# Performance work log

Hardware: AMD Instinct MI355X
Metric: run time of the kernel (lower is better)

Reference implementation:

```python
import jax, jax.numpy as jnp
import numpy as np

N = 50000        # nodes (== input_dim, featureless layer)
E = 400000       # edges in sparse support
HID = 200        # hidden dim hardcoded in GCN
NUM_CLASSES = 10


def setup_inputs() -> dict:
    key = jax.random.key(0)
    k1, k2, k3, k4 = jax.random.split(key, 4)
    return {
        "x": jnp.zeros((N, 1), dtype=jnp.float32),  # unused (featureless layer1)
        "support_rows": jax.random.randint(k1, (E,), 0, N, dtype=jnp.int32),
        "support_cols": jax.random.randint(k2, (E,), 0, N, dtype=jnp.int32),
        "support_vals": jax.random.uniform(k3, (E,), dtype=jnp.float32),
        "W0": jax.random.normal(k4, (N, HID), dtype=jnp.float32),
        "W2": jax.random.normal(jax.random.fold_in(key, 5), (HID, NUM_CLASSES), dtype=jnp.float32),
    }


def reference(x, support_rows, support_cols, support_vals, W0, W2):
    # Layer 1 (featureless): pre_sup = W0; out = A @ W0 via sparse edge list.
    # SpMM as gather + scale + segment-sum:
    gathered = W0[support_cols] * support_vals[:, None]          # [E, HID]
    h = jax.ops.segment_sum(gathered, support_rows, num_segments=N)  # [N, HID]
    h = jax.nn.relu(h)
    # Layer 2 (SimpleGraphConvolution, no act, no bias): h @ W2
    return h @ W2                                                # [N, NUM_CLASSES]
```

## Files before the change

kernel.cpp:

```cpp
#include <hip/hip_runtime.h>

#define N_NODES 50000
#define N_EDGES 400000
#define HID     200
#define NCLS    10
#define SLOTS   40


__device__ __forceinline__ unsigned bf16rn(float f) {
    unsigned u = __float_as_uint(f);
    return (u + 0x7FFFu + ((u >> 16) & 1u)) >> 16;
}
__device__ __forceinline__ float bl(unsigned u) { return __uint_as_float(u << 16); }
__device__ __forceinline__ float bh(unsigned u) { return __uint_as_float(u & 0xFFFF0000u); }

__global__ __launch_bounds__(256) void k_convert(const float4* __restrict__ W04,
                                                 uint4* __restrict__ W0h4,
                                                 int4* __restrict__ cnt4) {
    int i = blockIdx.x * 256 + threadIdx.x;
    if (i < 12504) cnt4[i] = make_int4(0, 0, 0, 0);
    if (i >= (N_NODES * HID) / 8) return;
    float4 f0 = W04[i * 2];
    float4 f1 = W04[i * 2 + 1];
    uint4 o;
    o.x = bf16rn(f0.x) | (bf16rn(f0.y) << 16);
    o.y = bf16rn(f0.z) | (bf16rn(f0.w) << 16);
    o.z = bf16rn(f1.x) | (bf16rn(f1.y) << 16);
    o.w = bf16rn(f1.z) | (bf16rn(f1.w) << 16);
    W0h4[i] = o;
}

__global__ void k_place(const int* __restrict__ rows, const int* __restrict__ cols,
                        const float* __restrict__ vals,
                        int* __restrict__ cnt, unsigned* __restrict__ ev) {
    int e = blockIdx.x * 256 + threadIdx.x;
    if (e >= N_EDGES) return;
    int r = rows[e];
    int pos = atomicAdd(&cnt[r], 1);
    if (pos < SLOTS)
        ev[(size_t)r * SLOTS + pos] = (bf16rn(vals[e]) << 16) | (unsigned)cols[e];
}

__global__ __launch_bounds__(256) void gcn_fused(
        const int*      __restrict__ cnt,
        const unsigned* __restrict__ ev,
        const ushort*   __restrict__ W0h,
        const float*    __restrict__ W2,
        float*          __restrict__ out) {
    __shared__ float w2p[25 * 81 + 7];
    {
        int t = threadIdx.x;
        if (t < HID) {
            float* dst = &w2p[(t >> 3) * 81 + (t & 7) * 10];
            const float* src = &W2[t * NCLS];
            *reinterpret_cast<float4*>(dst)     = *reinterpret_cast<const float4*>(src);
            *reinterpret_cast<float4*>(dst + 4) = *reinterpret_cast<const float4*>(src + 4);
            *reinterpret_cast<float2*>(dst + 8) = *reinterpret_cast<const float2*>(src + 8);
        }
    }
    __syncthreads();

    const int lane = threadIdx.x & 63;
    const int hl   = lane & 31;
    const bool selB = lane >= 32;
    const int lp   = min(hl, 24);
    const int off8 = lp * 8;
    const float* __restrict__ w2l = &w2p[lp * 81];

    const int w  = (blockIdx.x * 256 + threadIdx.x) >> 6;
    const int wu = __builtin_amdgcn_readfirstlane(w);

    const int2 cc = *reinterpret_cast<const int2*>(cnt + 2 * wu);
    const int nA = min(cc.x, SLOTS);
    const int nB = min(cc.y, SLOTS);
    const int n_my = selB ? nB : nA;
    const int nt = (max(nA, nB) + 7) >> 3;

    const unsigned* __restrict__ evp = ev + (size_t)(2 * wu) * SLOTS;

    float hk[8] = {0.f, 0.f, 0.f, 0.f, 0.f, 0.f, 0.f, 0.f};

    for (int t = 0; t < nt; ++t) {
        const int s = t * 8;
        const uint4 qa0 = *reinterpret_cast<const uint4*>(evp + s);
        const uint4 qa1 = *reinterpret_cast<const uint4*>(evp + s + 4);
        const uint4 qb0 = *reinterpret_cast<const uint4*>(evp + SLOTS + s);
        const uint4 qb1 = *reinterpret_cast<const uint4*>(evp + SLOTS + s + 4);

        unsigned q0 = selB ? qb0.x : qa0.x;
        unsigned q1 = selB ? qb0.y : qa0.y;
        unsigned q2 = selB ? qb0.z : qa0.z;
        unsigned q3 = selB ? qb0.w : qa0.w;
        unsigned q4 = selB ? qb1.x : qa1.x;
        unsigned q5 = selB ? qb1.y : qa1.y;
        unsigned q6 = selB ? qb1.z : qa1.z;
        unsigned q7 = selB ? qb1.w : qa1.w;
        q0 = (s + 0 < n_my) ? q0 : 0u;
        q1 = (s + 1 < n_my) ? q1 : 0u;
        q2 = (s + 2 < n_my) ? q2 : 0u;
        q3 = (s + 3 < n_my) ? q3 : 0u;
        q4 = (s + 4 < n_my) ? q4 : 0u;
        q5 = (s + 5 < n_my) ? q5 : 0u;
        q6 = (s + 6 < n_my) ? q6 : 0u;
        q7 = (s + 7 < n_my) ? q7 : 0u;

        uint4 g0 = *reinterpret_cast<const uint4*>(W0h + (size_t)(q0 & 0xFFFFu) * HID + off8);
        uint4 g1 = *reinterpret_cast<const uint4*>(W0h + (size_t)(q1 & 0xFFFFu) * HID + off8);
        uint4 g2 = *reinterpret_cast<const uint4*>(W0h + (size_t)(q2 & 0xFFFFu) * HID + off8);
        uint4 g3 = *reinterpret_cast<const uint4*>(W0h + (size_t)(q3 & 0xFFFFu) * HID + off8);
        uint4 g4 = *reinterpret_cast<const uint4*>(W0h + (size_t)(q4 & 0xFFFFu) * HID + off8);
        uint4 g5 = *reinterpret_cast<const uint4*>(W0h + (size_t)(q5 & 0xFFFFu) * HID + off8);
        uint4 g6 = *reinterpret_cast<const uint4*>(W0h + (size_t)(q6 & 0xFFFFu) * HID + off8);
        uint4 g7 = *reinterpret_cast<const uint4*>(W0h + (size_t)(q7 & 0xFFFFu) * HID + off8);

#define FMA8(g, q) {                                                    \
        float vv = bh(q);                                               \
        hk[0] += vv * bl((g).x);  hk[1] += vv * bh((g).x);              \
        hk[2] += vv * bl((g).y);  hk[3] += vv * bh((g).y);              \
        hk[4] += vv * bl((g).z);  hk[5] += vv * bh((g).z);              \
        hk[6] += vv * bl((g).w);  hk[7] += vv * bh((g).w); }
        FMA8(g0, q0); FMA8(g1, q1); FMA8(g2, q2); FMA8(g3, q3);
        FMA8(g4, q4); FMA8(g5, q5); FMA8(g6, q6); FMA8(g7, q7);
#undef FMA8
    }

    float xr[8];
#pragma unroll
    for (int j = 0; j < 8; ++j) xr[j] = fmaxf(hk[j], 0.f);

    float acc[NCLS];
#pragma unroll
    for (int c = 0; c < NCLS; ++c) acc[c] = 0.f;
#pragma unroll
    for (int j = 0; j < 8; ++j) {
#pragma unroll
        for (int c = 0; c < NCLS; ++c)
            acc[c] += xr[j] * w2l[j * 10 + c];
    }
    const float gate = (hl < 25) ? 1.f : 0.f;
#pragma unroll
    for (int c = 0; c < NCLS; ++c) acc[c] *= gate;

#pragma unroll
    for (int c = 0; c < NCLS; ++c) {
#pragma unroll
        for (int off = 16; off >= 1; off >>= 1)
            acc[c] += __shfl_xor(acc[c], off, 32);
    }

    if (lane == 0) {
        float* o = out + (size_t)(2 * w) * NCLS;
        *reinterpret_cast<float4*>(o)     = make_float4(acc[0], acc[1], acc[2], acc[3]);
        *reinterpret_cast<float4*>(o + 4) = make_float4(acc[4], acc[5], acc[6], acc[7]);
        *reinterpret_cast<float2*>(o + 8) = make_float2(acc[8], acc[9]);
    } else if (lane == 32) {
        float* o = out + (size_t)(2 * w + 1) * NCLS;
#pragma unroll
        for (int c = 0; c < NCLS; c += 2)
            *reinterpret_cast<float2*>(o + c) = make_float2(acc[c], acc[c + 1]);
    }
}

extern "C" void kernel_launch(void* const* d_in, const int* in_sizes, int n_in,
                              void* d_out, int out_size, void* d_ws, size_t ws_size,
                              hipStream_t stream) {
    const int*   rows = (const int*)  d_in[1];
    const int*   cols = (const int*)  d_in[2];
    const float* vals = (const float*)d_in[3];
    const float* W0   = (const float*)d_in[4];
    const float* W2   = (const float*)d_in[5];
    float*       out  = (float*)d_out;

    char* ws = (char*)d_ws;
    int*      cnt = (int*)     (ws);
    unsigned* ev  = (unsigned*)(ws + 200064);
    ushort*   W0h = (ushort*)  (ws + 8200064);

    int blocksC = ((N_NODES * HID) / 8 + 255) / 256;
    int blocksE = (N_EDGES + 255) / 256;

    k_convert<<<blocksC, 256, 0, stream>>>((const float4*)W0, (uint4*)W0h, (int4*)cnt);
    k_place  <<<blocksE, 256, 0, stream>>>(rows, cols, vals, cnt, ev);

    gcn_fused<<<6250, 256, 0, stream>>>(cnt, ev, W0h, W2, out);
}
```

Measured before the change: 80.54 us.

## Merge convert and place kernels, process four rows per wave

The W0 bf16 conversion and the edge placement are merged into one launch with block-range dispatch, and the counter zeroing moves to hipMemsetAsync. In the main kernel each wave now handles four rows instead of two, issuing twice as many independent gathers per iteration and halving the grid. It also adds a launch-bounds occupancy hint. The costs are higher register pressure, a padding loop driven by the maximum of four row lengths, and an extra memset call.

New measurement: 77.66 us. 1.04x faster.

```diff
diff --git a/kernel.cpp b/kernel.cpp
--- a/kernel.cpp
+++ b/kernel.cpp
@@ -6,6 +6,9 @@
 #define NCLS    10
 #define SLOTS   40
 
+#define BLOCKS_C 4883
+#define BLOCKS_E 1563
+
 
 __device__ __forceinline__ unsigned bf16rn(float f) {
     unsigned u = __float_as_uint(f);
@@ -14,34 +17,34 @@
 __device__ __forceinline__ float bl(unsigned u) { return __uint_as_float(u << 16); }
 __device__ __forceinline__ float bh(unsigned u) { return __uint_as_float(u & 0xFFFF0000u); }
 
-__global__ __launch_bounds__(256) void k_convert(const float4* __restrict__ W04,
-                                                 uint4* __restrict__ W0h4,
-                                                 int4* __restrict__ cnt4) {
-    int i = blockIdx.x * 256 + threadIdx.x;
-    if (i < 12504) cnt4[i] = make_int4(0, 0, 0, 0);
-    if (i >= (N_NODES * HID) / 8) return;
-    float4 f0 = W04[i * 2];
-    float4 f1 = W04[i * 2 + 1];
-    uint4 o;
-    o.x = bf16rn(f0.x) | (bf16rn(f0.y) << 16);
-    o.y = bf16rn(f0.z) | (bf16rn(f0.w) << 16);
-    o.z = bf16rn(f1.x) | (bf16rn(f1.y) << 16);
-    o.w = bf16rn(f1.z) | (bf16rn(f1.w) << 16);
-    W0h4[i] = o;
-}
-
-__global__ void k_place(const int* __restrict__ rows, const int* __restrict__ cols,
-                        const float* __restrict__ vals,
-                        int* __restrict__ cnt, unsigned* __restrict__ ev) {
-    int e = blockIdx.x * 256 + threadIdx.x;
-    if (e >= N_EDGES) return;
-    int r = rows[e];
-    int pos = atomicAdd(&cnt[r], 1);
-    if (pos < SLOTS)
-        ev[(size_t)r * SLOTS + pos] = (bf16rn(vals[e]) << 16) | (unsigned)cols[e];
-}
-
-__global__ __launch_bounds__(256) void gcn_fused(
+__global__ __launch_bounds__(256) void k_build(
+        const float4* __restrict__ W04, uint4* __restrict__ W0h4,
+        const int* __restrict__ rows, const int* __restrict__ cols,
+        const float* __restrict__ vals,
+        int* __restrict__ cnt, unsigned* __restrict__ ev) {
+    const int b = blockIdx.x;
+    if (b < BLOCKS_C) {
+        int i = b * 256 + threadIdx.x;
+        if (i >= (N_NODES * HID) / 8) return;
+        float4 f0 = W04[i * 2];
+        float4 f1 = W04[i * 2 + 1];
+        uint4 o;
+        o.x = bf16rn(f0.x) | (bf16rn(f0.y) << 16);
+        o.y = bf16rn(f0.z) | (bf16rn(f0.w) << 16);
+        o.z = bf16rn(f1.x) | (bf16rn(f1.y) << 16);
+        o.w = bf16rn(f1.z) | (bf16rn(f1.w) << 16);
+        W0h4[i] = o;
+    } else {
+        int e = (b - BLOCKS_C) * 256 + threadIdx.x;
+        if (e >= N_EDGES) return;
+        int r = rows[e];
+        int pos = atomicAdd(&cnt[r], 1);
+        if (pos < SLOTS)
+            ev[(size_t)r * SLOTS + pos] = (bf16rn(vals[e]) << 16) | (unsigned)cols[e];
+    }
+}
+
+__global__ __launch_bounds__(256, 4) void gcn_fused(
         const int*      __restrict__ cnt,
         const unsigned* __restrict__ ev,
         const ushort*   __restrict__ W0h,
@@ -70,94 +73,110 @@
     const int w  = (blockIdx.x * 256 + threadIdx.x) >> 6;
     const int wu = __builtin_amdgcn_readfirstlane(w);
 
-    const int2 cc = *reinterpret_cast<const int2*>(cnt + 2 * wu);
-    const int nA = min(cc.x, SLOTS);
-    const int nB = min(cc.y, SLOTS);
-    const int n_my = selB ? nB : nA;
-    const int nt = (max(nA, nB) + 7) >> 3;
-
-    const unsigned* __restrict__ evp = ev + (size_t)(2 * wu) * SLOTS;
-
-    float hk[8] = {0.f, 0.f, 0.f, 0.f, 0.f, 0.f, 0.f, 0.f};
-
-    for (int t = 0; t < nt; ++t) {
+    const int4 cc = *reinterpret_cast<const int4*>(cnt + 4 * wu);
+    const int nA = min(cc.x, SLOTS), nB = min(cc.y, SLOTS);
+    const int nC = min(cc.z, SLOTS), nD = min(cc.w, SLOTS);
+    const int n0 = selB ? nC : nA;
+    const int n1 = selB ? nD : nB;
+    const int ntm = (max(max(nA, nB), max(nC, nD)) + 7) >> 3;
+
+    const unsigned* __restrict__ evp = ev + (size_t)(4 * wu) * SLOTS;
+
+    float hk0[8] = {0.f, 0.f, 0.f, 0.f, 0.f, 0.f, 0.f, 0.f};
+    float hk1[8] = {0.f, 0.f, 0.f, 0.f, 0.f, 0.f, 0.f, 0.f};
+
+    for (int t = 0; t < ntm; ++t) {
         const int s = t * 8;
-        const uint4 qa0 = *reinterpret_cast<const uint4*>(evp + s);
-        const uint4 qa1 = *reinterpret_cast<const uint4*>(evp + s + 4);
-        const uint4 qb0 = *reinterpret_cast<const uint4*>(evp + SLOTS + s);
-        const uint4 qb1 = *reinterpret_cast<const uint4*>(evp + SLOTS + s + 4);
-
-        unsigned q0 = selB ? qb0.x : qa0.x;
-        unsigned q1 = selB ? qb0.y : qa0.y;
-        unsigned q2 = selB ? qb0.z : qa0.z;
-        unsigned q3 = selB ? qb0.w : qa0.w;
-        unsigned q4 = selB ? qb1.x : qa1.x;
-        unsigned q5 = selB ? qb1.y : qa1.y;
-        unsigned q6 = selB ? qb1.z : qa1.z;
-        unsigned q7 = selB ? qb1.w : qa1.w;
-        q0 = (s + 0 < n_my) ? q0 : 0u;
-        q1 = (s + 1 < n_my) ? q1 : 0u;
-        q2 = (s + 2 < n_my) ? q2 : 0u;
-        q3 = (s + 3 < n_my) ? q3 : 0u;
-        q4 = (s + 4 < n_my) ? q4 : 0u;
-        q5 = (s + 5 < n_my) ? q5 : 0u;
-        q6 = (s + 6 < n_my) ? q6 : 0u;
-        q7 = (s + 7 < n_my) ? q7 : 0u;
-
-        uint4 g0 = *reinterpret_cast<const uint4*>(W0h + (size_t)(q0 & 0xFFFFu) * HID + off8);
-        uint4 g1 = *reinterpret_cast<const uint4*>(W0h + (size_t)(q1 & 0xFFFFu) * HID + off8);
-        uint4 g2 = *reinterpret_cast<const uint4*>(W0h + (size_t)(q2 & 0xFFFFu) * HID + off8);
-        uint4 g3 = *reinterpret_cast<const uint4*>(W0h + (size_t)(q3 & 0xFFFFu) * HID + off8);
-        uint4 g4 = *reinterpret_cast<const uint4*>(W0h + (size_t)(q4 & 0xFFFFu) * HID + off8);
-        uint4 g5 = *reinterpret_cast<const uint4*>(W0h + (size_t)(q5 & 0xFFFFu) * HID + off8);
-        uint4 g6 = *reinterpret_cast<const uint4*>(W0h + (size_t)(q6 & 0xFFFFu) * HID + off8);
-        uint4 g7 = *reinterpret_cast<const uint4*>(W0h + (size_t)(q7 & 0xFFFFu) * HID + off8);
-
-#define FMA8(g, q) {                                                    \
+        const uint4 a0 = *reinterpret_cast<const uint4*>(evp + s);
+        const uint4 a1 = *reinterpret_cast<const uint4*>(evp + s + 4);
+        const uint4 b0 = *reinterpret_cast<const uint4*>(evp + SLOTS + s);
+        const uint4 b1 = *reinterpret_cast<const uint4*>(evp + SLOTS + s + 4);
+        const uint4 c0 = *reinterpret_cast<const uint4*>(evp + 2 * SLOTS + s);
+        const uint4 c1 = *reinterpret_cast<const uint4*>(evp + 2 * SLOTS + s + 4);
+        const uint4 d0 = *reinterpret_cast<const uint4*>(evp + 3 * SLOTS + s);
+        const uint4 d1 = *reinterpret_cast<const uint4*>(evp + 3 * SLOTS + s + 4);
+
+        unsigned u0 = (s + 0 < n0) ? (selB ? c0.x : a0.x) : 0u;
+        unsigned u1 = (s + 1 < n0) ? (selB ? c0.y : a0.y) : 0u;
+        unsigned u2 = (s + 2 < n0) ? (selB ? c0.z : a0.z) : 0u;
+        unsigned u3 = (s + 3 < n0) ? (selB ? c0.w : a0.w) : 0u;
+        unsigned u4 = (s + 4 < n0) ? (selB ? c1.x : a1.x) : 0u;
+        unsigned u5 = (s + 5 < n0) ? (selB ? c1.y : a1.y) : 0u;
+        unsigned u6 = (s + 6 < n0) ? (selB ? c1.z : a1.z) : 0u;
+        unsigned u7 = (s + 7 < n0) ? (selB ? c1.w : a1.w) : 0u;
+        unsigned v0 = (s + 0 < n1) ? (selB ? d0.x : b0.x) : 0u;
+        unsigned v1 = (s + 1 < n1) ? (selB ? d0.y : b0.y) : 0u;
+        unsigned v2 = (s + 2 < n1) ? (selB ? d0.z : b0.z) : 0u;
+        unsigned v3 = (s + 3 < n1) ? (selB ? d0.w : b0.w) : 0u;
+        unsigned v4 = (s + 4 < n1) ? (selB ? d1.x : b1.x) : 0u;
+        unsigned v5 = (s + 5 < n1) ? (selB ? d1.y : b1.y) : 0u;
+        unsigned v6 = (s + 6 < n1) ? (selB ? d1.z : b1.z) : 0u;
+        unsigned v7 = (s + 7 < n1) ? (selB ? d1.w : b1.w) : 0u;
+
+        uint4 gA0 = *reinterpret_cast<const uint4*>(W0h + (size_t)(u0 & 0xFFFFu) * HID + off8);
+        uint4 gA1 = *reinterpret_cast<const uint4*>(W0h + (size_t)(u1 & 0xFFFFu) * HID + off8);
+        uint4 gA2 = *reinterpret_cast<const uint4*>(W0h + (size_t)(u2 & 0xFFFFu) * HID + off8);
+        uint4 gA3 = *reinterpret_cast<const uint4*>(W0h + (size_t)(u3 & 0xFFFFu) * HID + off8);
+        uint4 gA4 = *reinterpret_cast<const uint4*>(W0h + (size_t)(u4 & 0xFFFFu) * HID + off8);
+        uint4 gA5 = *reinterpret_cast<const uint4*>(W0h + (size_t)(u5 & 0xFFFFu) * HID + off8);
+        uint4 gA6 = *reinterpret_cast<const uint4*>(W0h + (size_t)(u6 & 0xFFFFu) * HID + off8);
+        uint4 gA7 = *reinterpret_cast<const uint4*>(W0h + (size_t)(u7 & 0xFFFFu) * HID + off8);
+        uint4 gB0 = *reinterpret_cast<const uint4*>(W0h + (size_t)(v0 & 0xFFFFu) * HID + off8);
+        uint4 gB1 = *reinterpret_cast<const uint4*>(W0h + (size_t)(v1 & 0xFFFFu) * HID + off8);
+        uint4 gB2 = *reinterpret_cast<const uint4*>(W0h + (size_t)(v2 & 0xFFFFu) * HID + off8);
+        uint4 gB3 = *reinterpret_cast<const uint4*>(W0h + (size_t)(v3 & 0xFFFFu) * HID + off8);
+        uint4 gB4 = *reinterpret_cast<const uint4*>(W0h + (size_t)(v4 & 0xFFFFu) * HID + off8);
+        uint4 gB5 = *reinterpret_cast<const uint4*>(W0h + (size_t)(v5 & 0xFFFFu) * HID + off8);
+        uint4 gB6 = *reinterpret_cast<const uint4*>(W0h + (size_t)(v6 & 0xFFFFu) * HID + off8);
+        uint4 gB7 = *reinterpret_cast<const uint4*>(W0h + (size_t)(v7 & 0xFFFFu) * HID + off8);
+
+#define FMA8(H, g, q) {                                                 \
         float vv = bh(q);                                               \
-        hk[0] += vv * bl((g).x);  hk[1] += vv * bh((g).x);              \
-        hk[2] += vv * bl((g).y);  hk[3] += vv * bh((g).y);              \
-        hk[4] += vv * bl((g).z);  hk[5] += vv * bh((g).z);              \
-        hk[6] += vv * bl((g).w);  hk[7] += vv * bh((g).w); }
-        FMA8(g0, q0); FMA8(g1, q1); FMA8(g2, q2); FMA8(g3, q3);
-        FMA8(g4, q4); FMA8(g5, q5); FMA8(g6, q6); FMA8(g7, q7);
+        H[0] += vv * bl((g).x);  H[1] += vv * bh((g).x);                \
+        H[2] += vv * bl((g).y);  H[3] += vv * bh((g).y);                \
+        H[4] += vv * bl((g).z);  H[5] += vv * bh((g).z);                \
+        H[6] += vv * bl((g).w);  H[7] += vv * bh((g).w); }
+        FMA8(hk0, gA0, u0); FMA8(hk0, gA1, u1); FMA8(hk0, gA2, u2); FMA8(hk0, gA3, u3);
+        FMA8(hk0, gA4, u4); FMA8(hk0, gA5, u5); FMA8(hk0, gA6, u6); FMA8(hk0, gA7, u7);
+        FMA8(hk1, gB0, v0); FMA8(hk1, gB1, v1); FMA8(hk1, gB2, v2); FMA8(hk1, gB3, v3);
+        FMA8(hk1, gB4, v4); FMA8(hk1, gB5, v5); FMA8(hk1, gB6, v6); FMA8(hk1, gB7, v7);
 #undef FMA8
     }
 
-    float xr[8];
-#pragma unroll
-    for (int j = 0; j < 8; ++j) xr[j] = fmaxf(hk[j], 0.f);
-
-    float acc[NCLS];
-#pragma unroll
-    for (int c = 0; c < NCLS; ++c) acc[c] = 0.f;
+    float acc0[NCLS], acc1[NCLS];
+#pragma unroll
+    for (int c = 0; c < NCLS; ++c) { acc0[c] = 0.f; acc1[c] = 0.f; }
 #pragma unroll
     for (int j = 0; j < 8; ++j) {
-#pragma unroll
-        for (int c = 0; c < NCLS; ++c)
-            acc[c] += xr[j] * w2l[j * 10 + c];
+        float x0 = fmaxf(hk0[j], 0.f);
+        float x1 = fmaxf(hk1[j], 0.f);
+#pragma unroll
+        for (int c = 0; c < NCLS; ++c) {
+            float wv = w2l[j * 10 + c];
+            acc0[c] += x0 * wv;
+            acc1[c] += x1 * wv;
+        }
     }
     const float gate = (hl < 25) ? 1.f : 0.f;
 #pragma unroll
-    for (int c = 0; c < NCLS; ++c) acc[c] *= gate;
+    for (int c = 0; c < NCLS; ++c) { acc0[c] *= gate; acc1[c] *= gate; }
 
 #pragma unroll
     for (int c = 0; c < NCLS; ++c) {
 #pragma unroll
-        for (int off = 16; off >= 1; off >>= 1)
-            acc[c] += __shfl_xor(acc[c], off, 32);
-    }
-
-    if (lane == 0) {
-        float* o = out + (size_t)(2 * w) * NCLS;
-        *reinterpret_cast<float4*>(o)     = make_float4(acc[0], acc[1], acc[2], acc[3]);
-        *reinterpret_cast<float4*>(o + 4) = make_float4(acc[4], acc[5], acc[6], acc[7]);
-        *reinterpret_cast<float2*>(o + 8) = make_float2(acc[8], acc[9]);
-    } else if (lane == 32) {
-        float* o = out + (size_t)(2 * w + 1) * NCLS;
-#pragma unroll
-        for (int c = 0; c < NCLS; c += 2)
-            *reinterpret_cast<float2*>(o + c) = make_float2(acc[c], acc[c + 1]);
+        for (int off = 16; off >= 1; off >>= 1) {
+            acc0[c] += __shfl_xor(acc0[c], off, 32);
+            acc1[c] += __shfl_xor(acc1[c], off, 32);
+        }
+    }
+
+    if (hl == 0) {
+        float* o = out + (size_t)(4 * w + (selB ? 2 : 0)) * NCLS;
+        *reinterpret_cast<float4*>(o)      = make_float4(acc0[0], acc0[1], acc0[2], acc0[3]);
+        *reinterpret_cast<float4*>(o + 4)  = make_float4(acc0[4], acc0[5], acc0[6], acc0[7]);
+        *reinterpret_cast<float4*>(o + 8)  = make_float4(acc0[8], acc0[9], acc1[0], acc1[1]);
+        *reinterpret_cast<float4*>(o + 12) = make_float4(acc1[2], acc1[3], acc1[4], acc1[5]);
+        *reinterpret_cast<float4*>(o + 16) = make_float4(acc1[6], acc1[7], acc1[8], acc1[9]);
     }
 }
 
@@ -176,11 +195,10 @@
     unsigned* ev  = (unsigned*)(ws + 200064);
     ushort*   W0h = (ushort*)  (ws + 8200064);
 
-    int blocksC = ((N_NODES * HID) / 8 + 255) / 256;
-    int blocksE = (N_EDGES + 255) / 256;
-
-    k_convert<<<blocksC, 256, 0, stream>>>((const float4*)W0, (uint4*)W0h, (int4*)cnt);
-    k_place  <<<blocksE, 256, 0, stream>>>(rows, cols, vals, cnt, ev);
-
-    gcn_fused<<<6250, 256, 0, stream>>>(cnt, ev, W0h, W2, out);
-}
+    hipMemsetAsync(cnt, 0, 200064, stream);
+
+    k_build<<<BLOCKS_C + BLOCKS_E, 256, 0, stream>>>(
+        (const float4*)W0, (uint4*)W0h, rows, cols, vals, cnt, ev);
+
+    gcn_fused<<<3125, 256, 0, stream>>>(cnt, ev, W0h, W2, out);
+}
```
